# Kernel tuning notes

Hardware: AMD Instinct MI355X
Metric: run time of the kernel (lower is better)

The kernel has to match this reference:

```python
import jax, jax.numpy as jnp
import numpy as np

MAG = 1.0
TAU = 0.5
B, D, C = 8192, 256, 128


def setup_inputs() -> dict:
    key = jax.random.key(0)
    k1, k2 = jax.random.split(key)
    outputs = jax.random.normal(k1, (B, D), dtype=jnp.float32)
    labels = jax.random.normal(k2, (B, C), dtype=jnp.float32)
    return {"outputs": outputs, "labels": labels}


def reference(outputs, labels):
    # Cosine-similarity matrix of labels, min-max normalized to [0, 1]
    norm2labels = labels / (jnp.linalg.norm(labels, axis=1, keepdims=True) + 1e-12)
    sim_mat = norm2labels @ norm2labels.T  # [B, B]
    sim_mat = (sim_mat - sim_mat.min()) / (sim_mat.max() - sim_mat.min())

    # Pairwise Euclidean distances of outputs via the Gram trick
    # ||x_i - x_j||^2 = ||x_i||^2 + ||x_j||^2 - 2 <x_i, x_j>
    sq = jnp.sum(outputs * outputs, axis=1)  # [B]
    d2 = sq[:, None] + sq[None, :] - 2.0 * (outputs @ outputs.T)  # [B, B]
    d2 = jnp.maximum(d2, 0.0)
    nz = d2 > 0.0
    # safe sqrt: zero (diagonal) entries get distance 0 with zero gradient,
    # matching torch.norm's subgradient at 0
    eud = jnp.sqrt(jnp.where(nz, d2, 1.0)) * nz
    eud = eud / eud.max()

    distance = eud + sim_mat  # [B, B]
    pos_mask = sim_mat > TAU

    # Per-row masked log-sum-exp terms (distance in [0, 2], no overflow risk)
    pos_loss = jnp.log(jnp.sum(jnp.where(pos_mask, jnp.exp(distance), 0.0), axis=1))
    neg_loss = jnp.log(jnp.sum(jnp.where(pos_mask, 0.0, jnp.exp(MAG - distance)), axis=1))

    # clamp negatives (and -inf from empty masks) to 0, as the original `if < 0` does
    loss = jnp.maximum(pos_loss, 0.0) + jnp.maximum(neg_loss, 0.0)
    return jnp.mean(loss)
```

## Files before the change

### kernel.cpp

```cpp
#include <hip/hip_runtime.h>
#include <hip/hip_bf16.h>


#define B_N 8192
#define NT   64
#define TILE 128
#define NTRI 2080

typedef __attribute__((ext_vector_type(8))) short bf16x8;
typedef __attribute__((ext_vector_type(4))) float f32x4;

__device__ __forceinline__ unsigned fenc(float f) {
    unsigned u = __float_as_uint(f);
    return (u & 0x80000000u) ? ~u : (u | 0x80000000u);
}
__device__ __forceinline__ float fdec(unsigned k) {
    unsigned u = (k & 0x80000000u) ? (k ^ 0x80000000u) : ~k;
    return __uint_as_float(u);
}

__device__ __forceinline__ void tri_decode_swz(int b, int& bi, int& bj) {
    int t = (b & 7) * (NTRI / 8) + (b >> 3);
    int i = 0, rem = t;
    while (rem >= NT - i) { rem -= NT - i; i++; }
    bi = i; bj = i + rem;
}

__global__ __launch_bounds__(256) void prep_kernel(
    const float* __restrict__ outputs, const float* __restrict__ labels,
    __hip_bfloat16* __restrict__ Obp, __hip_bfloat16* __restrict__ Lnp,
    float* __restrict__ sq, float* __restrict__ pos_sums,
    float* __restrict__ neg_sums, unsigned* __restrict__ stats) {
    int w = threadIdx.x >> 6, lane = threadIdx.x & 63;
    int r = blockIdx.x * 4 + w;
    int g = r >> 4, rr = r & 15;

    f32x4 v = ((const f32x4*)outputs)[r * 64 + lane];
    float s = v[0]*v[0] + v[1]*v[1] + v[2]*v[2] + v[3]*v[3];
    #pragma unroll
    for (int m = 1; m < 64; m <<= 1) s += __shfl_xor(s, m);
    if (lane == 0) { sq[r] = s; pos_sums[r] = 0.f; neg_sums[r] = 0.f; }
    __hip_bfloat16 o4[4];
    #pragma unroll
    for (int i = 0; i < 4; i++) o4[i] = __float2bfloat16(v[i]);
    {
        int o = lane >> 1, pos = 4 * (lane & 1);
        size_t S = ((size_t)g * 32 + o) * 16 + rr;
        *(uint2*)&Obp[S * 8 + pos] = *(uint2*)o4;
    }

    float2 lv = ((const float2*)labels)[r * 64 + lane];
    float ls = lv.x * lv.x + lv.y * lv.y;
    #pragma unroll
    for (int m = 1; m < 64; m <<= 1) ls += __shfl_xor(ls, m);
    float nrm = sqrtf(ls) + 1e-12f;
    __hip_bfloat16 l2[2] = { __float2bfloat16(lv.x / nrm),
                             __float2bfloat16(lv.y / nrm) };
    {
        int o = lane >> 2, pos = 2 * (lane & 3);
        size_t S = ((size_t)g * 16 + o) * 16 + rr;
        *(unsigned*)&Lnp[S * 8 + pos] = *(unsigned*)l2;
    }

    if (blockIdx.x == 0 && threadIdx.x == 0) {
        stats[0] = 0xFFFFFFFFu; stats[1] = 0u; stats[2] = 0u;
    }
}

template<int KD8>
__device__ __forceinline__ void gram_packed(
    const short* __restrict__ P, int rb16, int cb16, int lane,
    f32x4 (&acc)[4][4]) {
    #pragma unroll
    for (int mi = 0; mi < 4; mi++)
        #pragma unroll
        for (int ni = 0; ni < 4; ni++) {
            f32x4 z = {0.f, 0.f, 0.f, 0.f};
            acc[mi][ni] = z;
        }
    #pragma unroll
    for (int kc = 0; kc < KD8 / 4; kc++) {
        bf16x8 a[4], b[4];
        #pragma unroll
        for (int mi = 0; mi < 4; mi++)
            a[mi] = *(const bf16x8*)&P[((size_t)(rb16 + mi) * KD8 * 16
                                        + kc * 64 + lane) * 8];
        #pragma unroll
        for (int ni = 0; ni < 4; ni++)
            b[ni] = *(const bf16x8*)&P[((size_t)(cb16 + ni) * KD8 * 16
                                        + kc * 64 + lane) * 8];
        #pragma unroll
        for (int mi = 0; mi < 4; mi++)
            #pragma unroll
            for (int ni = 0; ni < 4; ni++)
                acc[mi][ni] = __builtin_amdgcn_mfma_f32_16x16x32_bf16(
                    a[mi], b[ni], acc[mi][ni], 0, 0, 0);
    }
}

__global__ __launch_bounds__(256, 3) void stats_kernel(
    const short* __restrict__ Lnp, const short* __restrict__ Obp,
    const float* __restrict__ sq, unsigned* __restrict__ stats) {
    int bi, bj;
    tri_decode_swz(blockIdx.x, bi, bj);
    int tid = threadIdx.x, lane = tid & 63, wid = tid >> 6;
    int wm = (wid >> 1) * 64, wn = (wid & 1) * 64;
    int l15 = lane & 15, quad = lane >> 4;
    int rb16 = bi * 8 + (wid >> 1) * 4, cb16 = bj * 8 + (wid & 1) * 4;
    int rB = bi * TILE, cB = bj * TILE;

    float lmin = 1e30f, lmax = -1e30f, dmax = 0.f;
    f32x4 acc[4][4];

    gram_packed<16>(Lnp, rb16, cb16, lane, acc);
    #pragma unroll
    for (int mi = 0; mi < 4; mi++)
        #pragma unroll
        for (int ni = 0; ni < 4; ni++)
            #pragma unroll
            for (int r = 0; r < 4; r++) {
                float s = acc[mi][ni][r];
                lmin = fminf(lmin, s);
                lmax = fmaxf(lmax, s);
            }

    gram_packed<32>(Obp, rb16, cb16, lane, acc);
    float sqj[4];
    #pragma unroll
    for (int ni = 0; ni < 4; ni++) sqj[ni] = sq[cB + wn + ni * 16 + l15];
    #pragma unroll
    for (int mi = 0; mi < 4; mi++) {
        f32x4 sqi = *(const f32x4*)&sq[rB + wm + mi * 16 + quad * 4];
        #pragma unroll
        for (int r = 0; r < 4; r++)
            #pragma unroll
            for (int ni = 0; ni < 4; ni++) {
                float d2 = fmaxf(sqi[r] + sqj[ni] - 2.f * acc[mi][ni][r], 0.f);
                dmax = fmaxf(dmax, d2);
            }
    }

    #pragma unroll
    for (int m = 1; m < 64; m <<= 1) {
        lmin = fminf(lmin, __shfl_xor(lmin, m));
        lmax = fmaxf(lmax, __shfl_xor(lmax, m));
        dmax = fmaxf(dmax, __shfl_xor(dmax, m));
    }
    __shared__ float red[3][4];
    if ((tid & 63) == 0) { red[0][wid] = lmin; red[1][wid] = lmax; red[2][wid] = dmax; }
    __syncthreads();
    if (tid == 0) {
        lmin = fminf(fminf(red[0][0], red[0][1]), fminf(red[0][2], red[0][3]));
        lmax = fmaxf(fmaxf(red[1][0], red[1][1]), fmaxf(red[1][2], red[1][3]));
        dmax = fmaxf(fmaxf(red[2][0], red[2][1]), fmaxf(red[2][2], red[2][3]));
        atomicMin(&stats[0], fenc(lmin));
        atomicMax(&stats[1], fenc(lmax));
        atomicMax(&stats[2], fenc(dmax));
    }
}

__global__ __launch_bounds__(256, 2) void loss_kernel(
    const short* __restrict__ Lnp, const short* __restrict__ Obp,
    const float* __restrict__ sq, const unsigned* __restrict__ stats,
    float* __restrict__ pos_sums, float* __restrict__ neg_sums) {
    int bi, bj;
    tri_decode_swz(blockIdx.x, bi, bj);
    int tid = threadIdx.x, lane = tid & 63, wid = tid >> 6;
    int wm = (wid >> 1) * 64, wn = (wid & 1) * 64;
    int l15 = lane & 15, quad = lane >> 4;
    int rb16 = bi * 8 + (wid >> 1) * 4, cb16 = bj * 8 + (wid & 1) * 4;
    int rB = bi * TILE, cB = bj * TILE;

    __shared__ float rP[TILE][2], rN[TILE][2];
    __shared__ float cP[TILE][2], cN[TILE][2];

    f32x4 accS[4][4], accG[4][4];
    gram_packed<16>(Lnp, rb16, cb16, lane, accS);
    gram_packed<32>(Obp, rb16, cb16, lane, accG);

    float smin = fdec(stats[0]);
    float smax = fdec(stats[1]);
    float d2max = fdec(stats[2]);
    float invr = 1.f / (smax - smin);
    float invem = rsqrtf(d2max);

    float sqj[4];
    #pragma unroll
    for (int ni = 0; ni < 4; ni++) sqj[ni] = sq[cB + wn + ni * 16 + l15];
    float cpsum[4] = {0.f, 0.f, 0.f, 0.f};
    float cnsum[4] = {0.f, 0.f, 0.f, 0.f};

    #pragma unroll
    for (int mi = 0; mi < 4; mi++) {
        f32x4 sqi = *(const f32x4*)&sq[rB + wm + mi * 16 + quad * 4];
        float ps[4] = {0.f, 0.f, 0.f, 0.f};
        float ns[4] = {0.f, 0.f, 0.f, 0.f};
        #pragma unroll
        for (int ni = 0; ni < 4; ni++) {
            #pragma unroll
            for (int r = 0; r < 4; r++) {
                float sn = (accS[mi][ni][r] - smin) * invr;
                float g = accG[mi][ni][r];
                float d2 = fmaxf(sqi[r] + sqj[ni] - 2.f * g, 0.f);
                float eud = (d2 > 0.f) ? sqrtf(d2) * invem : 0.f;
                float dist = eud + sn;
                bool pos = sn > 0.5f;
                float pv = pos ? __expf(dist) : 0.f;
                float nv = pos ? 0.f : __expf(1.0f - dist);
                ps[r] += pv;  ns[r] += nv;
                cpsum[ni] += pv;  cnsum[ni] += nv;
            }
        }
        #pragma unroll
        for (int r = 0; r < 4; r++) {
            #pragma unroll
            for (int m = 1; m < 16; m <<= 1) {
                ps[r] += __shfl_xor(ps[r], m);
                ns[r] += __shfl_xor(ns[r], m);
            }
            if (l15 == 0) {
                int rr = wm + mi * 16 + quad * 4 + r;
                rP[rr][wid & 1] = ps[r];
                rN[rr][wid & 1] = ns[r];
            }
        }
    }
    #pragma unroll
    for (int ni = 0; ni < 4; ni++) {
        #pragma unroll
        for (int m = 16; m < 64; m <<= 1) {
            cpsum[ni] += __shfl_xor(cpsum[ni], m);
            cnsum[ni] += __shfl_xor(cnsum[ni], m);
        }
        if (quad == 0) {
            int cc = wn + ni * 16 + l15;
            cP[cc][wid >> 1] = cpsum[ni];
            cN[cc][wid >> 1] = cnsum[ni];
        }
    }
    __syncthreads();
    if (tid < TILE) {
        atomicAdd(&pos_sums[bi * TILE + tid], rP[tid][0] + rP[tid][1]);
        atomicAdd(&neg_sums[bi * TILE + tid], rN[tid][0] + rN[tid][1]);
        if (bi != bj) {
            atomicAdd(&pos_sums[bj * TILE + tid], cP[tid][0] + cP[tid][1]);
            atomicAdd(&neg_sums[bj * TILE + tid], cN[tid][0] + cN[tid][1]);
        }
    }
}

__global__ __launch_bounds__(256) void finalize_kernel(
    const float* __restrict__ pos_sums, const float* __restrict__ neg_sums,
    float* __restrict__ out) {
    int t = threadIdx.x;
    float acc = 0.f;
    for (int i = t; i < B_N; i += 256) {
        float p = pos_sums[i], n = neg_sums[i];
        float pl = fmaxf(logf(p), 0.f);
        float nl = (n > 0.f) ? fmaxf(logf(n), 0.f) : 0.f;
        acc += pl + nl;
    }
    #pragma unroll
    for (int m = 1; m < 64; m <<= 1) acc += __shfl_xor(acc, m);
    __shared__ float w4[4];
    if ((t & 63) == 0) w4[t >> 6] = acc;
    __syncthreads();
    if (t == 0) out[0] = (w4[0] + w4[1] + w4[2] + w4[3]) / (float)B_N;
}

extern "C" void kernel_launch(void* const* d_in, const int* in_sizes, int n_in,
                              void* d_out, int out_size, void* d_ws, size_t ws_size,
                              hipStream_t stream) {
    const float* outputs = (const float*)d_in[0];
    const float* labels  = (const float*)d_in[1];
    float* out = (float*)d_out;
    char* ws = (char*)d_ws;
    __hip_bfloat16* Obp = (__hip_bfloat16*)(ws);
    __hip_bfloat16* Lnp = (__hip_bfloat16*)(ws + 4194304);
    float* sq           = (float*)(ws + 6291456);
    float* pos_sums     = (float*)(ws + 6324224);
    float* neg_sums     = (float*)(ws + 6356992);
    unsigned* stats     = (unsigned*)(ws + 6389760);

    prep_kernel<<<B_N / 4, 256, 0, stream>>>(outputs, labels, Obp, Lnp, sq,
                                             pos_sums, neg_sums, stats);
    stats_kernel<<<NTRI, 256, 0, stream>>>((const short*)Lnp, (const short*)Obp,
                                           sq, stats);
    loss_kernel<<<NTRI, 256, 0, stream>>>((const short*)Lnp, (const short*)Obp,
                                          sq, stats, pos_sums, neg_sums);
    finalize_kernel<<<1, 256, 0, stream>>>(pos_sums, neg_sums, out);
}
```

Baseline: 251.5 us.

## Supertile block ordering, LDS-staged packed prep, raise loss kernel occupancy

Replaces the swizzled triangular tile decode with a two-level supertile ordering. Blocks first walk the 16x16 diagonal supertiles and then the off-diagonal ones, so that concurrently running blocks share row and column panels in cache. The prep kernel now handles 16 rows per block and stages the bf16 data in LDS, so the packed layout is written with coalesced 16-byte stores instead of scattered small ones. The loss kernel's launch bounds move from 2 to 3 blocks per CU, which may force register spills.

```diff
diff --git a/kernel.cpp b/kernel.cpp
--- a/kernel.cpp
+++ b/kernel.cpp
@@ -19,11 +19,21 @@
     return __uint_as_float(u);
 }
 
-__device__ __forceinline__ void tri_decode_swz(int b, int& bi, int& bj) {
-    int t = (b & 7) * (NTRI / 8) + (b >> 3);
-    int i = 0, rem = t;
-    while (rem >= NT - i) { rem -= NT - i; i++; }
-    bi = i; bj = i + rem;
+__device__ __forceinline__ void tile_decode(int b, int& bi, int& bj) {
+    int si, sj, ti, tj;
+    if (b < 544) {
+        int sb = b / 136, w = b - sb * 136;
+        int i = 0;
+        while (w >= 16 - i) { w -= 16 - i; i++; }
+        si = sb; sj = sb; ti = i; tj = i + w;
+    } else {
+        int q = (b - 544) >> 8, w = (b - 544) & 255;
+        int i = 0;
+        while (q >= 3 - i) { q -= 3 - i; i++; }
+        si = i; sj = i + 1 + q;
+        ti = w >> 4; tj = w & 15;
+    }
+    bi = si * 16 + ti; bj = sj * 16 + tj;
 }
 
 __global__ __launch_bounds__(256) void prep_kernel(
@@ -31,39 +41,60 @@
     __hip_bfloat16* __restrict__ Obp, __hip_bfloat16* __restrict__ Lnp,
     float* __restrict__ sq, float* __restrict__ pos_sums,
     float* __restrict__ neg_sums, unsigned* __restrict__ stats) {
-    int w = threadIdx.x >> 6, lane = threadIdx.x & 63;
-    int r = blockIdx.x * 4 + w;
-    int g = r >> 4, rr = r & 15;
-
-    f32x4 v = ((const f32x4*)outputs)[r * 64 + lane];
-    float s = v[0]*v[0] + v[1]*v[1] + v[2]*v[2] + v[3]*v[3];
-    #pragma unroll
-    for (int m = 1; m < 64; m <<= 1) s += __shfl_xor(s, m);
-    if (lane == 0) { sq[r] = s; pos_sums[r] = 0.f; neg_sums[r] = 0.f; }
-    __hip_bfloat16 o4[4];
-    #pragma unroll
-    for (int i = 0; i < 4; i++) o4[i] = __float2bfloat16(v[i]);
+    int g = blockIdx.x, tid = threadIdx.x;
+    int rl = tid >> 4, c = tid & 15;
+    int row = g * 16 + rl;
+    __shared__ __align__(16) short tO[16][264];
+    __shared__ __align__(16) short tL[16][136];
+
+    float s = 0.f;
+    #pragma unroll
+    for (int k = 0; k < 4; k++) {
+        f32x4 v = *(const f32x4*)&outputs[(size_t)row * 256 + c * 16 + k * 4];
+        s += v[0]*v[0] + v[1]*v[1] + v[2]*v[2] + v[3]*v[3];
+        __hip_bfloat16 b4[4];
+        #pragma unroll
+        for (int i = 0; i < 4; i++) b4[i] = __float2bfloat16(v[i]);
+        *(uint2*)&tO[rl][c * 16 + k * 4] = *(uint2*)b4;
+    }
+    #pragma unroll
+    for (int m = 1; m < 16; m <<= 1) s += __shfl_xor(s, m);
+    if (c == 0) sq[row] = s;
+
+    float ls = 0.f;
+    f32x4 u0 = *(const f32x4*)&labels[(size_t)row * 128 + c * 8];
+    f32x4 u1 = *(const f32x4*)&labels[(size_t)row * 128 + c * 8 + 4];
+    ls += u0[0]*u0[0] + u0[1]*u0[1] + u0[2]*u0[2] + u0[3]*u0[3];
+    ls += u1[0]*u1[0] + u1[1]*u1[1] + u1[2]*u1[2] + u1[3]*u1[3];
+    #pragma unroll
+    for (int m = 1; m < 16; m <<= 1) ls += __shfl_xor(ls, m);
+    float inv = 1.f / (sqrtf(ls) + 1e-12f);
     {
-        int o = lane >> 1, pos = 4 * (lane & 1);
-        size_t S = ((size_t)g * 32 + o) * 16 + rr;
-        *(uint2*)&Obp[S * 8 + pos] = *(uint2*)o4;
-    }
-
-    float2 lv = ((const float2*)labels)[r * 64 + lane];
-    float ls = lv.x * lv.x + lv.y * lv.y;
-    #pragma unroll
-    for (int m = 1; m < 64; m <<= 1) ls += __shfl_xor(ls, m);
-    float nrm = sqrtf(ls) + 1e-12f;
-    __hip_bfloat16 l2[2] = { __float2bfloat16(lv.x / nrm),
-                             __float2bfloat16(lv.y / nrm) };
+        __hip_bfloat16 b4[4];
+        #pragma unroll
+        for (int i = 0; i < 4; i++) b4[i] = __float2bfloat16(u0[i] * inv);
+        *(uint2*)&tL[rl][c * 8] = *(uint2*)b4;
+        #pragma unroll
+        for (int i = 0; i < 4; i++) b4[i] = __float2bfloat16(u1[i] * inv);
+        *(uint2*)&tL[rl][c * 8 + 4] = *(uint2*)b4;
+    }
+    if (tid < 16) { pos_sums[g * 16 + tid] = 0.f; neg_sums[g * 16 + tid] = 0.f; }
+    if (g == 0 && tid == 0) {
+        stats[0] = 0xFFFFFFFFu; stats[1] = 0u; stats[2] = 0u;
+    }
+    __syncthreads();
+
+    #pragma unroll
+    for (int q = 0; q < 2; q++) {
+        int sl = tid * 2 + q;
+        int o = sl >> 4, rr = sl & 15;
+        uint4 d = *(uint4*)&tO[rr][o * 8];
+        *(uint4*)&Obp[(size_t)g * 4096 + (size_t)sl * 8] = d;
+    }
     {
-        int o = lane >> 2, pos = 2 * (lane & 3);
-        size_t S = ((size_t)g * 16 + o) * 16 + rr;
-        *(unsigned*)&Lnp[S * 8 + pos] = *(unsigned*)l2;
-    }
-
-    if (blockIdx.x == 0 && threadIdx.x == 0) {
-        stats[0] = 0xFFFFFFFFu; stats[1] = 0u; stats[2] = 0u;
+        int o = tid >> 4, rr = tid & 15;
+        uint4 d = *(uint4*)&tL[rr][o * 8];
+        *(uint4*)&Lnp[(size_t)g * 2048 + (size_t)tid * 8] = d;
     }
 }
 
@@ -102,7 +133,7 @@
     const short* __restrict__ Lnp, const short* __restrict__ Obp,
     const float* __restrict__ sq, unsigned* __restrict__ stats) {
     int bi, bj;
-    tri_decode_swz(blockIdx.x, bi, bj);
+    tile_decode(blockIdx.x, bi, bj);
     int tid = threadIdx.x, lane = tid & 63, wid = tid >> 6;
     int wm = (wid >> 1) * 64, wn = (wid & 1) * 64;
     int l15 = lane & 15, quad = lane >> 4;
@@ -159,12 +190,12 @@
     }
 }
 
-__global__ __launch_bounds__(256, 2) void loss_kernel(
+__global__ __launch_bounds__(256, 3) void loss_kernel(
     const short* __restrict__ Lnp, const short* __restrict__ Obp,
     const float* __restrict__ sq, const unsigned* __restrict__ stats,
     float* __restrict__ pos_sums, float* __restrict__ neg_sums) {
     int bi, bj;
-    tri_decode_swz(blockIdx.x, bi, bj);
+    tile_decode(blockIdx.x, bi, bj);
     int tid = threadIdx.x, lane = tid & 63, wid = tid >> 6;
     int wm = (wid >> 1) * 64, wn = (wid & 1) * 64;
     int l15 = lane & 15, quad = lane >> 4;
@@ -282,8 +313,8 @@
     float* neg_sums     = (float*)(ws + 6356992);
     unsigned* stats     = (unsigned*)(ws + 6389760);
 
-    prep_kernel<<<B_N / 4, 256, 0, stream>>>(outputs, labels, Obp, Lnp, sq,
-                                             pos_sums, neg_sums, stats);
+    prep_kernel<<<B_N / 16, 256, 0, stream>>>(outputs, labels, Obp, Lnp, sq,
+                                              pos_sums, neg_sums, stats);
     stats_kernel<<<NTRI, 256, 0, stream>>>((const short*)Lnp, (const short*)Obp,
                                            sq, stats);
     loss_kernel<<<NTRI, 256, 0, stream>>>((const short*)Lnp, (const short*)Obp,
```

Result: no change. 249.5 us (-0.8%).
